# Optimization experiments

Measured on AMD Instinct MI355X. Metric: run time of the kernel, lower is better.

The kernel has to match this reference:

```python
import jax, jax.numpy as jnp
import numpy as np

DIM = 64
NUM_GRAPHS = 256
SLOPE = 11.0 / 48.0  # RReLU eval slope = ((1/8)+(1/3))/2
EPS = 1e-5


def _bn(x, g, b):
    m = x.mean(0)
    v = x.var(0)  # biased, matches torch BN normalization
    return (x - m) * jax.lax.rsqrt(v + EPS) * g + b


def _rrelu(x):
    return jnp.where(x >= 0, x, SLOPE * x)


def _gru(x, h, Wih, Whh, bih, bhh):
    gi = x @ Wih.T + bih
    gh = h @ Whh.T + bhh
    ir, iz, inn = jnp.split(gi, 3, -1)
    hr, hz, hn = jnp.split(gh, 3, -1)
    r = jax.nn.sigmoid(ir + hr)
    z = jax.nn.sigmoid(iz + hz)
    n = jnp.tanh(inn + r * hn)
    return (1.0 - z) * n + z * h


def _nnconv(x, ei, We, bias, n_nodes):
    # edge-conditioned conv: gather src, per-edge matmul, scatter-mean to dst
    src, dst = ei[0], ei[1]
    msg = jnp.einsum('ei,eio->eo', x[src], We)
    s = jax.ops.segment_sum(msg, dst, num_segments=n_nodes)
    cnt = jax.ops.segment_sum(jnp.ones((ei.shape[1],), x.dtype), dst, num_segments=n_nodes)
    return s / jnp.maximum(cnt, 1.0)[:, None] + bias


def _seg_softmax(e, seg, nseg):
    m = jax.ops.segment_max(e, seg, num_segments=nseg)
    ex = jnp.exp(e - m[seg])
    den = jax.ops.segment_sum(ex, seg, num_segments=nseg)
    return ex / den[seg]


def _set2set(x, seg, nseg, Wih, Whh, bih, bhh, steps=3):
    H = x.shape[-1]
    q_star = jnp.zeros((nseg, 2 * H), x.dtype)
    h = jnp.zeros((nseg, H), x.dtype)
    c = jnp.zeros((nseg, H), x.dtype)
    for _ in range(steps):
        gates = q_star @ Wih.T + bih + h @ Whh.T + bhh
        i, f, g, o = jnp.split(gates, 4, -1)
        c = jax.nn.sigmoid(f) * c + jax.nn.sigmoid(i) * jnp.tanh(g)
        h = jax.nn.sigmoid(o) * jnp.tanh(c)
        e = jnp.sum(x * h[seg], -1)
        a = _seg_softmax(e, seg, nseg)
        r = jax.ops.segment_sum(a[:, None] * x, seg, num_segments=nseg)
        q_star = jnp.concatenate([h, r], -1)
    return q_star


def reference(x, edge_index, edge_attr, edge_index3, edge_attr3, batch,
              bnx_g, bnx_b, Wn, bnode, We, be, Wnn1, bias1,
              Wih1, Whh1, bih1, bhh1, bnc_g, bnc_b, Wc1, bc1, Wc2, bc2,
              Wnn2, bias2, Wih2, Whh2, bih2, bhh2,
              Ws_ih, Ws_hh, bs_ih, bs_hh, bno_g, bno_b, Ww, Wb):
    N = x.shape[0]
    out = _rrelu(_bn(x, bnx_g, bnx_b) @ Wn + bnode)          # [N, 64]
    ea = _rrelu(edge_attr @ We + be)                          # [E, 12]
    W1 = (ea @ Wnn1).reshape(-1, DIM, DIM)                    # [E, 64, 64]
    h = out
    for _ in range(2):
        m = _rrelu(_nnconv(out, edge_index, W1, bias1, N))
        h = _gru(m, h, Wih1, Whh1, bih1, bhh1)
        out = h
    out = _bn(out, bnc_g, bnc_b)
    out = _rrelu(out @ Wc1 + bc1)
    out = _rrelu(out @ Wc2 + bc2)                             # [N, 128] (dropout=identity in eval)
    ei3s = jnp.concatenate([edge_index3, edge_index3[::-1]], axis=1)
    ea3s = jnp.concatenate([edge_attr3, edge_attr3], axis=0)
    W2 = (ea3s @ Wnn2).reshape(-1, 2 * DIM, 2 * DIM)          # [2*E3, 128, 128]
    h = out
    for _ in range(2):
        m = _rrelu(_nnconv(out, ei3s, W2, bias2, N))
        h = _gru(m, h, Wih2, Whh2, bih2, bhh2)
        out = h
    cbi = batch[edge_index3[0]]
    pool = _set2set(out, batch, NUM_GRAPHS, Ws_ih, Ws_hh, bs_ih, bs_hh)[cbi]
    t0 = out[edge_index3[0]]
    t1 = out[edge_index3[1]]
    yhat = jnp.concatenate([(t0 + t1) * 0.5, t0 * t1, (t0 - t1) ** 2, pool], axis=1)  # [E3, 640]
    yhat = _bn(yhat, bno_g, bno_b)
    w = edge_attr3 @ Ww
    b = edge_attr3 @ Wb
    return jnp.sum(yhat * w, axis=1) + b[:, 0]


def setup_inputs() -> dict:
    key = jax.random.key(0)
    ks = iter(jax.random.split(key, 64))
    def nrm(shape, scale=1.0):
        return jax.random.normal(next(ks), shape, jnp.float32) * scale
    def lin(i, o):
        return nrm((i, o), 1.0 / np.sqrt(i))
    N, E, E3 = 8192, 16384, 1024
    inp = {}
    inp['x'] = nrm((N, 8))
    inp['edge_index'] = jax.random.randint(next(ks), (2, E), 0, N)
    inp['edge_attr'] = nrm((E, 19))
    inp['edge_index3'] = jax.random.randint(next(ks), (2, E3), 0, N)
    inp['edge_attr3'] = nrm((E3, 8))
    inp['batch'] = jnp.repeat(jnp.arange(NUM_GRAPHS), N // NUM_GRAPHS)
    inp['bnx_g'] = jnp.ones(8); inp['bnx_b'] = jnp.zeros(8)
    inp['Wn'] = lin(8, 64); inp['bnode'] = jnp.zeros(64)
    inp['We'] = lin(19, 12); inp['be'] = jnp.zeros(12)
    inp['Wnn1'] = lin(12, DIM * DIM) * 0.5; inp['bias1'] = jnp.zeros(64)
    inp['Wih1'] = nrm((192, 64), 1.0 / np.sqrt(64)); inp['Whh1'] = nrm((192, 64), 1.0 / np.sqrt(64))
    inp['bih1'] = jnp.zeros(192); inp['bhh1'] = jnp.zeros(192)
    inp['bnc_g'] = jnp.ones(64); inp['bnc_b'] = jnp.zeros(64)
    inp['Wc1'] = lin(64, 128); inp['bc1'] = jnp.zeros(128)
    inp['Wc2'] = lin(128, 128); inp['bc2'] = jnp.zeros(128)
    inp['Wnn2'] = lin(8, 4 * DIM * DIM) * 0.5; inp['bias2'] = jnp.zeros(128)
    inp['Wih2'] = nrm((384, 128), 1.0 / np.sqrt(128)); inp['Whh2'] = nrm((384, 128), 1.0 / np.sqrt(128))
    inp['bih2'] = jnp.zeros(384); inp['bhh2'] = jnp.zeros(384)
    inp['Ws_ih'] = nrm((512, 256), 1.0 / np.sqrt(256)); inp['Ws_hh'] = nrm((512, 128), 1.0 / np.sqrt(128))
    inp['bs_ih'] = jnp.zeros(512); inp['bs_hh'] = jnp.zeros(512)
    inp['bno_g'] = jnp.ones(640); inp['bno_b'] = jnp.zeros(640)
    inp['Ww'] = lin(8, 640); inp['Wb'] = lin(8, 1)
    return inp
```

## Files before the change

kernel.cpp:

```cpp
#include <hip/hip_runtime.h>
#include <hip/hip_bf16.h>
#include <math.h>

#define N_NODES 8192
#define N_EDGES 16384
#define N_E3    1024
#define NGRAPH  256
#define NPG     32
#define SLOPE   (11.0f/48.0f)
#define BN_EPS  1e-5f

__device__ __forceinline__ float rrelu(float v){ return v >= 0.f ? v : SLOPE*v; }
__device__ __forceinline__ float sigm(float v){ return 1.f/(1.f+__expf(-v)); }

typedef _Float16 f16;
typedef __attribute__((ext_vector_type(8))) _Float16 half8v;
typedef __attribute__((ext_vector_type(4))) float f32x4;

__device__ __forceinline__ void zero_tail(int zb, float* zptr, int zcount) {
  float4 z4 = make_float4(0.f,0.f,0.f,0.f);
  int bd = blockDim.x;
  for (int i = zb*bd + (int)threadIdx.x; i*4 < zcount; i += 16*bd)
    ((float4*)zptr)[i] = z4;
}

__global__ __launch_bounds__(256) void conv1f_k(const float* __restrict__ nodeA,
    const int* __restrict__ ei, const float* __restrict__ ea,
    const f16* __restrict__ Wz1h, float* __restrict__ sbuf) {
  int t = threadIdx.x, lane = t & 63, wv = t >> 6;
  int e0 = blockIdx.x*64 + wv*16;
  int eA = e0 + (lane & 15);
  int src = ei[eA];
  int kb0 = (lane >> 4) * 8;
  const float* ap = nodeA + (size_t)src*64 + kb0;
  float4 v0 = *(const float4*)ap,      v1 = *(const float4*)(ap+4);
  float4 v2 = *(const float4*)(ap+32), v3 = *(const float4*)(ap+36);
  half8v a0, a1;
  a0[0]=(f16)v0.x; a0[1]=(f16)v0.y; a0[2]=(f16)v0.z; a0[3]=(f16)v0.w;
  a0[4]=(f16)v1.x; a0[5]=(f16)v1.y; a0[6]=(f16)v1.z; a0[7]=(f16)v1.w;
  a1[0]=(f16)v2.x; a1[1]=(f16)v2.y; a1[2]=(f16)v2.z; a1[3]=(f16)v2.w;
  a1[4]=(f16)v3.x; a1[5]=(f16)v3.y; a1[6]=(f16)v3.z; a1[7]=(f16)v3.w;
  float eav[12];
  #pragma unroll
  for (int kg = 0; kg < 12; kg++) eav[kg] = ea[eA*12 + kg];

  f32x4 acc[4] = {{0,0,0,0},{0,0,0,0},{0,0,0,0},{0,0,0,0}};
  #pragma unroll
  for (int kg = 0; kg < 12; kg++) {
    f16 s = (f16)eav[kg];
    half8v s0, s1;
    #pragma unroll
    for (int u = 0; u < 8; u++) { s0[u] = a0[u]*s; s1[u] = a1[u]*s; }
    #pragma unroll
    for (int jf = 0; jf < 4; jf++) {
      const f16* wp = Wz1h + (size_t)(kg*64 + jf*16 + (lane & 15))*64 + kb0;
      acc[jf] = __builtin_amdgcn_mfma_f32_16x16x32_f16(s0, *(const half8v*)wp, acc[jf], 0, 0, 0);
      acc[jf] = __builtin_amdgcn_mfma_f32_16x16x32_f16(s1, *(const half8v*)(wp+32), acc[jf], 0, 0, 0);
    }
  }
  int dstv[4];
  #pragma unroll
  for (int r = 0; r < 4; r++) dstv[r] = ei[N_EDGES + e0 + ((lane>>4)<<2) + r];
  #pragma unroll
  for (int jf = 0; jf < 4; jf++) {
    int col = jf*16 + (lane & 15);
    #pragma unroll
    for (int r = 0; r < 4; r++)
      atomicAdd(&sbuf[dstv[r]*64 + col], acc[jf][r]);
  }
}

__global__ __launch_bounds__(512) void conv2f_k(const float* __restrict__ nodeB,
    const int* __restrict__ ei3, const float* __restrict__ ea3,
    const f16* __restrict__ W2fh, float* __restrict__ sbuf) {
  int t = threadIdx.x, lane = t & 63, wv = t >> 6;
  int eg = blockIdx.x >> 1, qh = blockIdx.x & 1;
  int kgh = wv >> 2, jp = wv & 3;
  int e0 = eg * 16;
  int eA = e0 + (lane & 15);
  int src = ei3[eA];
  int kb0 = qh*64 + (lane >> 4) * 8;
  const float* ap = nodeB + (size_t)src*128 + kb0;
  half8v a0, a1;
  {
    float4 w0 = *(const float4*)ap,        w1 = *(const float4*)(ap+4);
    float4 w2 = *(const float4*)(ap + 32), w3 = *(const float4*)(ap+36);
    a0[0]=(f16)w0.x; a0[1]=(f16)w0.y; a0[2]=(f16)w0.z; a0[3]=(f16)w0.w;
    a0[4]=(f16)w1.x; a0[5]=(f16)w1.y; a0[6]=(f16)w1.z; a0[7]=(f16)w1.w;
    a1[0]=(f16)w2.x; a1[1]=(f16)w2.y; a1[2]=(f16)w2.z; a1[3]=(f16)w2.w;
    a1[4]=(f16)w3.x; a1[5]=(f16)w3.y; a1[6]=(f16)w3.z; a1[7]=(f16)w3.w;
  }
  int eb = eA & (N_E3 - 1);
  float eav[4];
  #pragma unroll
  for (int kk = 0; kk < 4; kk++) eav[kk] = ea3[eb*8 + kgh*4 + kk];

  f32x4 acc[2] = {{0,0,0,0},{0,0,0,0}};
  #pragma unroll
  for (int kk = 0; kk < 4; kk++) {
    f16 s = (f16)eav[kk];
    half8v s0, s1;
    #pragma unroll
    for (int u = 0; u < 8; u++) { s0[u] = a0[u]*s; s1[u] = a1[u]*s; }
    int kg = kgh*4 + kk;
    #pragma unroll
    for (int jj = 0; jj < 2; jj++) {
      int jf = jp*2 + jj;
      const f16* wp = W2fh + (size_t)(kg*128 + jf*16 + (lane & 15))*128 + kb0;
      acc[jj] = __builtin_amdgcn_mfma_f32_16x16x32_f16(s0, *(const half8v*)wp, acc[jj], 0, 0, 0);
      acc[jj] = __builtin_amdgcn_mfma_f32_16x16x32_f16(s1, *(const half8v*)(wp+32), acc[jj], 0, 0, 0);
    }
  }
  int dstv[4];
  #pragma unroll
  for (int r = 0; r < 4; r++) dstv[r] = ei3[(e0 + ((lane>>4)<<2) + r + N_E3) & (2*N_E3 - 1)];
  #pragma unroll
  for (int jj = 0; jj < 2; jj++) {
    int col = (jp*2+jj)*16 + (lane & 15);
    #pragma unroll
    for (int r = 0; r < 4; r++)
      atomicAdd(&sbuf[dstv[r]*128 + col], acc[jj][r]);
  }
}

template<int LOGH, int STATS>
__global__ void gruf_k(const float* __restrict__ sbuf, const float* __restrict__ cnt,
                       const float* __restrict__ mbias,
                       const f16* __restrict__ Wih, const f16* __restrict__ Whh,
                       const float* __restrict__ bih, const float* __restrict__ bhh,
                       const float* __restrict__ hold, float* __restrict__ hnew,
                       float* __restrict__ bns1, float* __restrict__ bns2,
                       int nblk, float* __restrict__ zptr, int zcount) {
  if ((int)blockIdx.x >= nblk) { zero_tail(blockIdx.x - nblk, zptr, zcount); return; }
  const int H = 1 << LOGH;
  const int K = H;
  const int jt = H >> 6;
  int t = threadIdx.x;
  int lane = t & 63, wv = t >> 6;
  int wpb = blockDim.x >> 6;
  int bm = blockIdx.x / jt, bj = blockIdx.x % jt;
  int n0 = bm * (wpb << 4) + (wv << 4);
  int j0 = bj << 6;
  int row = n0 + (lane & 15);
  int kb0 = (lane >> 4) * 8;

  f32x4 aR[4]  = {{0,0,0,0},{0,0,0,0},{0,0,0,0},{0,0,0,0}};
  f32x4 aZ[4]  = {{0,0,0,0},{0,0,0,0},{0,0,0,0},{0,0,0,0}};
  f32x4 aIN[4] = {{0,0,0,0},{0,0,0,0},{0,0,0,0},{0,0,0,0}};
  f32x4 aHN[4] = {{0,0,0,0},{0,0,0,0},{0,0,0,0},{0,0,0,0}};

  float dn = 1.f / fmaxf(cnt[row], 1.0f);
  for (int k0 = 0; k0 < K; k0 += 32) {
    int kb = k0 + kb0;
    const float* ap = sbuf + (size_t)row * K + kb;
    float4 v0 = *(const float4*)ap, v1 = *(const float4*)(ap + 4);
    float4 b0 = *(const float4*)(mbias + kb), b1 = *(const float4*)(mbias + kb + 4);
    half8v af;
    af[0]=(f16)rrelu(v0.x*dn+b0.x); af[1]=(f16)rrelu(v0.y*dn+b0.y);
    af[2]=(f16)rrelu(v0.z*dn+b0.z); af[3]=(f16)rrelu(v0.w*dn+b0.w);
    af[4]=(f16)rrelu(v1.x*dn+b1.x); af[5]=(f16)rrelu(v1.y*dn+b1.y);
    af[6]=(f16)rrelu(v1.z*dn+b1.z); af[7]=(f16)rrelu(v1.w*dn+b1.w);
    #pragma unroll
    for (int jf = 0; jf < 4; jf++) {
      int wr = j0 + jf*16 + (lane & 15);
      half8v wR = *(const half8v*)(Wih + (size_t)wr*K + kb);
      half8v wZ = *(const half8v*)(Wih + (size_t)(H + wr)*K + kb);
      half8v wN = *(const half8v*)(Wih + (size_t)(2*H + wr)*K + kb);
      aR[jf]  = __builtin_amdgcn_mfma_f32_16x16x32_f16(af, wR, aR[jf], 0, 0, 0);
      aZ[jf]  = __builtin_amdgcn_mfma_f32_16x16x32_f16(af, wZ, aZ[jf], 0, 0, 0);
      aIN[jf] = __builtin_amdgcn_mfma_f32_16x16x32_f16(af, wN, aIN[jf], 0, 0, 0);
    }
  }
  for (int k0 = 0; k0 < K; k0 += 32) {
    int kb = k0 + kb0;
    const float* ap = hold + (size_t)row * K + kb;
    float4 v0 = *(const float4*)ap, v1 = *(const float4*)(ap + 4);
    half8v af;
    af[0]=(f16)v0.x; af[1]=(f16)v0.y; af[2]=(f16)v0.z; af[3]=(f16)v0.w;
    af[4]=(f16)v1.x; af[5]=(f16)v1.y; af[6]=(f16)v1.z; af[7]=(f16)v1.w;
    #pragma unroll
    for (int jf = 0; jf < 4; jf++) {
      int wr = j0 + jf*16 + (lane & 15);
      half8v wR = *(const half8v*)(Whh + (size_t)wr*K + kb);
      half8v wZ = *(const half8v*)(Whh + (size_t)(H + wr)*K + kb);
      half8v wN = *(const half8v*)(Whh + (size_t)(2*H + wr)*K + kb);
      aR[jf]  = __builtin_amdgcn_mfma_f32_16x16x32_f16(af, wR, aR[jf], 0, 0, 0);
      aZ[jf]  = __builtin_amdgcn_mfma_f32_16x16x32_f16(af, wZ, aZ[jf], 0, 0, 0);
      aHN[jf] = __builtin_amdgcn_mfma_f32_16x16x32_f16(af, wN, aHN[jf], 0, 0, 0);
    }
  }
  int r0 = n0 + ((lane >> 4) << 2);
  #pragma unroll
  for (int jf = 0; jf < 4; jf++) {
    int col = j0 + jf*16 + (lane & 15);
    float bR = bih[col] + bhh[col];
    float bZ = bih[H + col] + bhh[H + col];
    float bI = bih[2*H + col], bH = bhh[2*H + col];
    float ssum = 0.f, sq = 0.f;
    #pragma unroll
    for (int r = 0; r < 4; r++) {
      float rr = sigm(aR[jf][r] + bR);
      float zz = sigm(aZ[jf][r] + bZ);
      float nn = tanhf(aIN[jf][r] + bI + rr*(aHN[jf][r] + bH));
      float ho = hold[(size_t)(r0 + r)*H + col];
      float hv = (1.f - zz)*nn + zz*ho;
      hnew[(size_t)(r0 + r)*H + col] = hv;
      if (STATS) { ssum += hv; sq += hv*hv; }
    }
    if (STATS) {
      ssum += __shfl_xor(ssum, 16); ssum += __shfl_xor(ssum, 32);
      sq   += __shfl_xor(sq, 16);   sq   += __shfl_xor(sq, 32);
      if (lane < 16) { atomicAdd(&bns1[col], ssum); atomicAdd(&bns2[col], sq); }
    }
  }
}

__global__ __launch_bounds__(256) void fcf_k(const float* __restrict__ A,
    const f16* __restrict__ W1, const float* __restrict__ b1v,
    const f16* __restrict__ W2, const float* __restrict__ b2v,
    const float* __restrict__ bns1, const float* __restrict__ bns2,
    const float* __restrict__ g, const float* __restrict__ b,
    float* __restrict__ outB,
    int nblk, float* __restrict__ zptr, int zcount) {
  if ((int)blockIdx.x >= nblk) { zero_tail(blockIdx.x - nblk, zptr, zcount); return; }
  __shared__ f16 y1s[4][16][128];
  int t = threadIdx.x, lane = t & 63, wv = t >> 6;
  int n0 = blockIdx.x*64 + wv*16;
  int row = n0 + (lane & 15);
  int kb0 = (lane >> 4) * 8;
  const float invN = 1.f / (float)N_NODES;

  const float* ap = A + (size_t)row*64 + kb0;
  half8v af0, af1;
  #pragma unroll
  for (int u = 0; u < 8; u++) {
    int k0i = kb0 + u, k1i = 32 + kb0 + u;
    float m0 = bns1[k0i]*invN, m1 = bns1[k1i]*invN;
    float va0 = bns2[k0i]*invN - m0*m0, va1 = bns2[k1i]*invN - m1*m1;
    af0[u] = (f16)((ap[u]    - m0)*rsqrtf(va0+BN_EPS)*g[k0i] + b[k0i]);
    af1[u] = (f16)((ap[32+u] - m1)*rsqrtf(va1+BN_EPS)*g[k1i] + b[k1i]);
  }
  f32x4 acc1[8] = {{0,0,0,0},{0,0,0,0},{0,0,0,0},{0,0,0,0},
                   {0,0,0,0},{0,0,0,0},{0,0,0,0},{0,0,0,0}};
  #pragma unroll
  for (int jf = 0; jf < 8; jf++) {
    const f16* wp = W1 + (size_t)(jf*16 + (lane & 15))*64 + kb0;
    acc1[jf] = __builtin_amdgcn_mfma_f32_16x16x32_f16(af0, *(const half8v*)wp, acc1[jf], 0, 0, 0);
    acc1[jf] = __builtin_amdgcn_mfma_f32_16x16x32_f16(af1, *(const half8v*)(wp+32), acc1[jf], 0, 0, 0);
  }
  #pragma unroll
  for (int jf = 0; jf < 8; jf++) {
    int col = jf*16 + (lane & 15);
    float bv = b1v[col];
    #pragma unroll
    for (int r = 0; r < 4; r++) {
      int rl = ((lane >> 4) << 2) + r;
      y1s[wv][rl][col] = (f16)rrelu(acc1[jf][r] + bv);
    }
  }
  __syncthreads();
  half8v bf[4];
  #pragma unroll
  for (int q = 0; q < 4; q++)
    bf[q] = *(const half8v*)&y1s[wv][lane & 15][q*32 + kb0];
  f32x4 acc2[8] = {{0,0,0,0},{0,0,0,0},{0,0,0,0},{0,0,0,0},
                   {0,0,0,0},{0,0,0,0},{0,0,0,0},{0,0,0,0}};
  #pragma unroll
  for (int jf = 0; jf < 8; jf++) {
    const f16* wp = W2 + (size_t)(jf*16 + (lane & 15))*128 + kb0;
    #pragma unroll
    for (int q = 0; q < 4; q++)
      acc2[jf] = __builtin_amdgcn_mfma_f32_16x16x32_f16(bf[q], *(const half8v*)(wp + q*32), acc2[jf], 0, 0, 0);
  }
  int r0 = n0 + ((lane >> 4) << 2);
  #pragma unroll
  for (int jf = 0; jf < 8; jf++) {
    int col = jf*16 + (lane & 15);
    float bv = b2v[col];
    #pragma unroll
    for (int r = 0; r < 4; r++)
      outB[(size_t)(r0 + r)*128 + col] = rrelu(acc2[jf][r] + bv);
  }
}

__global__ void bn_stats_k(const float* __restrict__ X, int nrow, int F,
                           float* __restrict__ mean, float* __restrict__ var) {
  int f = blockIdx.x, t = threadIdx.x;
  __shared__ float s1[256], s2[256];
  float a = 0.f, b = 0.f;
  for (int n = t; n < nrow; n += 256) {
    float v = X[(size_t)n * F + f];
    a += v; b += v * v;
  }
  s1[t] = a; s2[t] = b; __syncthreads();
  for (int w = 128; w > 0; w >>= 1) {
    if (t < w) { s1[t] += s1[t+w]; s2[t] += s2[t+w]; }
    __syncthreads();
  }
  if (t == 0) {
    float m = s1[0] / (float)nrow;
    mean[f] = m;
    var[f]  = s2[0] / (float)nrow - m * m;
  }
}

__global__ void embed_k(const float* __restrict__ x,
                        const float* __restrict__ mean, const float* __restrict__ var,
                        const float* __restrict__ g, const float* __restrict__ b,
                        const float* __restrict__ Wn, const float* __restrict__ bnode,
                        float* __restrict__ nodeA,
                        const float* __restrict__ eattr,
                        const float* __restrict__ We, const float* __restrict__ be,
                        float* __restrict__ ea12,
                        const int* __restrict__ ei, const int* __restrict__ ei3,
                        float* __restrict__ cnt1, float* __restrict__ cnt2,
                        float* __restrict__ zptr) {
  int bid = blockIdx.x, t = threadIdx.x;
  if (bid < 2048) {
    int idx = bid * 256 + t;
    int n = idx >> 6, o = idx & 63;
    float acc = bnode[o];
    #pragma unroll
    for (int i = 0; i < 8; i++) {
      float xn = (x[n*8+i] - mean[i]) * rsqrtf(var[i] + BN_EPS) * g[i] + b[i];
      acc += xn * Wn[i*64 + o];
    }
    nodeA[idx] = rrelu(acc);
  } else if (bid < 2816) {
    int idx = (bid - 2048) * 256 + t;
    if (idx >= N_EDGES * 12) return;
    int e = idx / 12, j = idx - e * 12;
    float acc = be[j];
    #pragma unroll
    for (int k = 0; k < 19; k++) acc += eattr[e*19+k] * We[k*12 + j];
    ea12[idx] = rrelu(acc);
  } else if (bid < 2880) {
    int idx = (bid - 2816) * 256 + t;
    if (idx < N_EDGES) atomicAdd(&cnt1[ei[N_EDGES + idx]], 1.0f);
    if (idx < N_E3) {
      atomicAdd(&cnt2[ei3[N_E3 + idx]], 1.0f);
      atomicAdd(&cnt2[ei3[idx]], 1.0f);
    }
  } else {
    zero_tail(bid - 2880, zptr, N_NODES*64);
  }
}

__global__ void pack_k(const float* __restrict__ Wnn1,
                       const float* __restrict__ Wih1, const float* __restrict__ Whh1,
                       const float* __restrict__ Wc1,  const float* __restrict__ Wc2,
                       const float* __restrict__ Wnn2,
                       const float* __restrict__ Wih2, const float* __restrict__ Whh2,
                       const float* __restrict__ Ws_ih, const float* __restrict__ Ws_hh,
                       f16* __restrict__ Wz1h,
                       f16* __restrict__ Wih1h, f16* __restrict__ Whh1h,
                       f16* __restrict__ Wc1Th, f16* __restrict__ Wc2Th,
                       f16* __restrict__ W2fh,
                       f16* __restrict__ Wih2h, f16* __restrict__ Whh2h,
                       float* __restrict__ Wfold,
                       float* __restrict__ cnt1, float* __restrict__ cnt2,
                       float* __restrict__ bns1, float* __restrict__ bns2) {
  int idx = blockIdx.x * 256 + threadIdx.x;
  if (idx < 49152) {
    int jj = idx >> 6, i = idx & 63;
    int k = jj >> 6, o = jj & 63;
    Wz1h[idx] = (f16)Wnn1[k*4096 + i*64 + o];
  }
  if (idx < 12288) { Wih1h[idx] = (f16)Wih1[idx]; Whh1h[idx] = (f16)Whh1[idx]; }
  if (idx < 8192) {
    int o = idx >> 6, i = idx & 63;
    Wc1Th[idx] = (f16)Wc1[i*128 + o];
  }
  if (idx < 16384) {
    int o = idx >> 7, i = idx & 127;
    Wc2Th[idx] = (f16)Wc2[i*128 + o];
  }
  if (idx < 131072) {
    int r = idx >> 7, i = idx & 127;
    int k = r >> 7, o = r & 127;
    W2fh[idx] = (f16)Wnn2[k*16384 + i*128 + o];
  }
  if (idx < 49152) { Wih2h[idx] = (f16)Wih2[idx]; Whh2h[idx] = (f16)Whh2[idx]; }
  if (idx < 131072) {
    int i = idx >> 9, j = idx & 511;
    float v = Ws_ih[(size_t)j*256 + i];
    if (i < 128) v += Ws_hh[(size_t)j*128 + i];
    Wfold[idx] = v;
  }
  if (idx < N_NODES) { cnt1[idx] = 0.f; cnt2[idx] = 0.f; }
  if (idx < 128) { bns1[idx] = 0.f; bns2[idx] = 0.f; }
}

__global__ __launch_bounds__(1024) void set2set_k(const float* __restrict__ x,
    const float* __restrict__ Wfold,
    const float* __restrict__ bs_ih, const float* __restrict__ bs_hh,
    float* __restrict__ qpool) {
  int g = blockIdx.x, t = threadIdx.x;
  __shared__ float xs[NPG*128];
  __shared__ float hr[256];
  __shared__ float cbuf[128];
  __shared__ float pbuf[1024];
  __shared__ float abuf[NPG];
  *(float4*)&xs[t*4] = *(const float4*)(x + (size_t)g*NPG*128 + t*4);
  if (t < 128) {
    float gi = bs_ih[t]     + bs_hh[t];
    float gg = bs_ih[256+t] + bs_hh[256+t];
    float go = bs_ih[384+t] + bs_hh[384+t];
    float c0 = sigm(gi) * tanhf(gg);
    cbuf[t] = c0;
    hr[t] = sigm(go) * tanhf(c0);
  }
  __syncthreads();
  #pragma unroll 1
  for (int step = 0; step < 3; step++) {
    {
      int node = t >> 5, s = t & 31;
      const float* xr = xs + node*128 + s*4;
      float p = xr[0]*hr[s*4] + xr[1]*hr[s*4+1] + xr[2]*hr[s*4+2] + xr[3]*hr[s*4+3];
      p += __shfl_down(p, 16, 32); p += __shfl_down(p, 8, 32);
      p += __shfl_down(p, 4, 32);  p += __shfl_down(p, 2, 32);
      p += __shfl_down(p, 1, 32);
      if (s == 0) pbuf[node] = p;
    }
    __syncthreads();
    if (t < NPG) {
      float e = pbuf[t];
      float mx = e;
      for (int o = 16; o > 0; o >>= 1) mx = fmaxf(mx, __shfl_xor(mx, o, 32));
      float ex = __expf(e - mx);
      float den = ex;
      for (int o = 16; o > 0; o >>= 1) den += __shfl_xor(den, o, 32);
      abuf[t] = ex / den;
    }
    __syncthreads();
    if (t < 128) {
      float r = 0.f;
      #pragma unroll 8
      for (int nn = 0; nn < NPG; nn++) r += abuf[nn] * xs[nn*128 + t];
      hr[128 + t] = r;
    }
    __syncthreads();
    if (step == 2) break;
    {
      int j = t & 511, half = t >> 9;
      const float* wp = Wfold + (size_t)(half*128)*512 + j;
      const float* iv = hr + half*128;
      float a0=0.f, a1=0.f, a2=0.f, a3=0.f;
      #pragma unroll 4
      for (int i = 0; i < 128; i += 4) {
        a0 += iv[i]   * wp[(i)  *512];
        a1 += iv[i+1] * wp[(i+1)*512];
        a2 += iv[i+2] * wp[(i+2)*512];
        a3 += iv[i+3] * wp[(i+3)*512];
      }
      pbuf[t] = a0 + a1 + a2 + a3;
    }
    __syncthreads();
    if (t < 128) {
      float gi = pbuf[t]     + pbuf[512+t] + bs_ih[t]     + bs_hh[t];
      float gf = pbuf[128+t] + pbuf[640+t] + bs_ih[128+t] + bs_hh[128+t];
      float gg = pbuf[256+t] + pbuf[768+t] + bs_ih[256+t] + bs_hh[256+t];
      float go = pbuf[384+t] + pbuf[896+t] + bs_ih[384+t] + bs_hh[384+t];
      float ci = sigm(gf) * cbuf[t] + sigm(gi) * tanhf(gg);
      cbuf[t] = ci;
      hr[t] = sigm(go) * tanhf(ci);
    }
    __syncthreads();
  }
  if (t < 256) qpool[g*256 + t] = hr[t];
}

__global__ void yhat_k(const float* __restrict__ feat, const int* __restrict__ ei3,
                       const int* __restrict__ batch, const float* __restrict__ qpool,
                       float* __restrict__ yhat) {
  int idx = blockIdx.x * blockDim.x + threadIdx.x;
  if (idx >= N_E3 * 640) return;
  int e = idx / 640, j = idx - e * 640;
  int s0 = ei3[e], s1 = ei3[N_E3 + e];
  float v;
  if (j < 128)      { v = 0.5f * (feat[s0*128+j] + feat[s1*128+j]); }
  else if (j < 256) { int jj = j-128; v = feat[s0*128+jj] * feat[s1*128+jj]; }
  else if (j < 384) { int jj = j-256; float d = feat[s0*128+jj] - feat[s1*128+jj]; v = d*d; }
  else              { int cbi = batch[s0]; v = qpool[cbi*256 + (j-384)]; }
  yhat[idx] = v;
}

__global__ void final_k(const float* __restrict__ yhat,
                        const float* __restrict__ mean, const float* __restrict__ var,
                        const float* __restrict__ g, const float* __restrict__ b,
                        const float* __restrict__ ea3,
                        const float* __restrict__ Ww, const float* __restrict__ Wb,
                        float* __restrict__ out) {
  int e = blockIdx.x, t = threadIdx.x;
  __shared__ float red[128];
  float av[8];
  #pragma unroll
  for (int k = 0; k < 8; k++) av[k] = ea3[e*8 + k];
  float acc = 0.f;
  for (int j = t; j < 640; j += 128) {
    float yn = (yhat[(size_t)e*640 + j] - mean[j]) * rsqrtf(var[j] + BN_EPS) * g[j] + b[j];
    float wj = 0.f;
    #pragma unroll
    for (int k = 0; k < 8; k++) wj += av[k] * Ww[k*640 + j];
    acc += yn * wj;
  }
  red[t] = acc; __syncthreads();
  for (int w = 64; w > 0; w >>= 1) {
    if (t < w) red[t] += red[t+w];
    __syncthreads();
  }
  if (t == 0) {
    float bb = 0.f;
    #pragma unroll
    for (int k = 0; k < 8; k++) bb += av[k] * Wb[k];
    out[e] = red[0] + bb;
  }
}

extern "C" void kernel_launch(void* const* d_in, const int* in_sizes, int n_in,
                              void* d_out, int out_size, void* d_ws, size_t ws_size,
                              hipStream_t stream) {
  const float* x      = (const float*)d_in[0];
  const int*   ei     = (const int*)  d_in[1];
  const float* eattr  = (const float*)d_in[2];
  const int*   ei3    = (const int*)  d_in[3];
  const float* ea3    = (const float*)d_in[4];
  const int*   batch  = (const int*)  d_in[5];
  const float* bnx_g  = (const float*)d_in[6];
  const float* bnx_b  = (const float*)d_in[7];
  const float* Wn     = (const float*)d_in[8];
  const float* bnode  = (const float*)d_in[9];
  const float* We     = (const float*)d_in[10];
  const float* be     = (const float*)d_in[11];
  const float* Wnn1   = (const float*)d_in[12];
  const float* bias1  = (const float*)d_in[13];
  const float* Wih1   = (const float*)d_in[14];
  const float* Whh1   = (const float*)d_in[15];
  const float* bih1   = (const float*)d_in[16];
  const float* bhh1   = (const float*)d_in[17];
  const float* bnc_g  = (const float*)d_in[18];
  const float* bnc_b  = (const float*)d_in[19];
  const float* Wc1    = (const float*)d_in[20];
  const float* bc1    = (const float*)d_in[21];
  const float* Wc2    = (const float*)d_in[22];
  const float* bc2    = (const float*)d_in[23];
  const float* Wnn2   = (const float*)d_in[24];
  const float* bias2  = (const float*)d_in[25];
  const float* Wih2   = (const float*)d_in[26];
  const float* Whh2   = (const float*)d_in[27];
  const float* bih2   = (const float*)d_in[28];
  const float* bhh2   = (const float*)d_in[29];
  const float* Ws_ih  = (const float*)d_in[30];
  const float* Ws_hh  = (const float*)d_in[31];
  const float* bs_ih  = (const float*)d_in[32];
  const float* bs_hh  = (const float*)d_in[33];
  const float* bno_g  = (const float*)d_in[34];
  const float* bno_b  = (const float*)d_in[35];
  const float* Ww     = (const float*)d_in[36];
  const float* Wb     = (const float*)d_in[37];
  float* out = (float*)d_out;

  float* W = (float*)d_ws;
  size_t off = 0;
  float* Wfold  = W + off; off += 131072;
  float* ea12   = W + off; off += (size_t)N_EDGES * 12;
  float* nodeA  = W + off; off += (size_t)N_NODES * 64;
  float* nodeA2 = W + off; off += (size_t)N_NODES * 64;
  float* sA1    = W + off; off += (size_t)N_NODES * 64;
  float* sA2    = W + off; off += (size_t)N_NODES * 64;
  float* sB1    = W + off; off += (size_t)N_NODES * 128;
  float* sB2    = W + off; off += (size_t)N_NODES * 128;
  float* cnt1   = W + off; off += (size_t)N_NODES;
  float* cnt2   = W + off; off += (size_t)N_NODES;
  float* nodeB  = W + off; off += (size_t)N_NODES * 128;
  float* nodeB2 = W + off; off += (size_t)N_NODES * 128;
  float* qpool  = W + off; off += (size_t)NGRAPH * 256;
  float* yhat   = W + off; off += (size_t)N_E3 * 640;
  float* mean   = W + off; off += 640;
  float* var    = W + off; off += 640;
  float* bns1   = W + off; off += 128;
  float* bns2   = W + off; off += 128;
  f16* F = (f16*)(W + off);
  size_t foff = 0;
  f16* Wz1h  = F + foff; foff += 49152;
  f16* Wih1h = F + foff; foff += 12288;
  f16* Whh1h = F + foff; foff += 12288;
  f16* Wc1Th = F + foff; foff += 8192;
  f16* Wc2Th = F + foff; foff += 16384;
  f16* W2fh  = F + foff; foff += 131072;
  f16* Wih2h = F + foff; foff += 49152;
  f16* Whh2h = F + foff; foff += 49152;
  (void)foff; (void)ws_size; (void)in_sizes; (void)n_in; (void)out_size;

  pack_k<<<512, 256, 0, stream>>>(Wnn1, Wih1, Whh1, Wc1, Wc2, Wnn2, Wih2, Whh2, Ws_ih, Ws_hh,
                                  Wz1h, Wih1h, Whh1h, Wc1Th, Wc2Th, W2fh, Wih2h, Whh2h,
                                  Wfold, cnt1, cnt2, bns1, bns2);
  bn_stats_k<<<8, 256, 0, stream>>>(x, N_NODES, 8, mean, var);
  embed_k<<<2896, 256, 0, stream>>>(x, mean, var, bnx_g, bnx_b, Wn, bnode, nodeA,
                                    eattr, We, be, ea12, ei, ei3, cnt1, cnt2, sA1);

  conv1f_k<<<256, 256, 0, stream>>>(nodeA, ei, ea12, Wz1h, sA1);
  gruf_k<6,0><<<272, 128, 0, stream>>>(sA1, cnt1, bias1, Wih1h, Whh1h, bih1, bhh1,
                                       nodeA, nodeA2, nullptr, nullptr,
                                       256, sA2, N_NODES*64);
  conv1f_k<<<256, 256, 0, stream>>>(nodeA2, ei, ea12, Wz1h, sA2);
  gruf_k<6,1><<<272, 128, 0, stream>>>(sA2, cnt1, bias1, Wih1h, Whh1h, bih1, bhh1,
                                       nodeA2, nodeA, bns1, bns2,
                                       256, sB1, N_NODES*128);

  fcf_k<<<144, 256, 0, stream>>>(nodeA, Wc1Th, bc1, Wc2Th, bc2,
                                 bns1, bns2, bnc_g, bnc_b, nodeB,
                                 128, sB2, N_NODES*128);

  conv2f_k<<<256, 512, 0, stream>>>(nodeB, ei3, ea3, W2fh, sB1);
  gruf_k<7,0><<<256, 256, 0, stream>>>(sB1, cnt2, bias2, Wih2h, Whh2h, bih2, bhh2,
                                       nodeB, nodeB2, nullptr, nullptr,
                                       256, nullptr, 0);
  conv2f_k<<<256, 512, 0, stream>>>(nodeB2, ei3, ea3, W2fh, sB2);
  gruf_k<7,0><<<256, 256, 0, stream>>>(sB2, cnt2, bias2, Wih2h, Whh2h, bih2, bhh2,
                                       nodeB2, nodeB, nullptr, nullptr,
                                       256, nullptr, 0);

  set2set_k<<<NGRAPH, 1024, 0, stream>>>(nodeB, Wfold, bs_ih, bs_hh, qpool);

  yhat_k<<<(N_E3*640 + 255)/256, 256, 0, stream>>>(nodeB, ei3, batch, qpool, yhat);
  bn_stats_k<<<640, 256, 0, stream>>>(yhat, N_E3, 640, mean, var);
  final_k<<<N_E3, 128, 0, stream>>>(yhat, mean, var, bno_g, bno_b, ea3, Ww, Wb, out);
}
```

Baseline: 198.7 us.

## Fuse pack, embed, conv and GRU stages into one cooperative persistent kernel

Replaces the chain of about eleven small launches (weight packing, BN stats, embedding, two conv1/GRU rounds, FC, two conv2/GRU rounds) with one cooperative kernel of 256 blocks of 512 threads that separates the stages with grid.sync. The goal is to remove kernel launch gaps and tail effects between many short stages. Work is remapped to fewer, larger blocks with 8 waves each, so some stages now run on only part of the grid. Grid-wide barriers carry their own cost, and the 512-thread blocks with launch_bounds(512,2) may limit register use for the MFMA bodies.

```diff
diff --git a/kernel.cpp b/kernel.cpp
--- a/kernel.cpp
+++ b/kernel.cpp
@@ -1,6 +1,9 @@
 #include <hip/hip_runtime.h>
+#include <hip/hip_cooperative_groups.h>
 #include <hip/hip_bf16.h>
 #include <math.h>
+
+namespace cg = cooperative_groups;
 
 #define N_NODES 8192
 #define N_EDGES 16384
@@ -17,18 +20,29 @@
 typedef __attribute__((ext_vector_type(8))) _Float16 half8v;
 typedef __attribute__((ext_vector_type(4))) float f32x4;
 
-__device__ __forceinline__ void zero_tail(int zb, float* zptr, int zcount) {
+struct P {
+  const float *x, *eattr, *ea3;
+  const int *ei, *ei3;
+  const float *bnx_g, *bnx_b, *Wn, *bnode, *We, *be;
+  const float *Wnn1, *bias1, *Wih1, *Whh1, *bih1, *bhh1;
+  const float *bnc_g, *bnc_b, *Wc1, *bc1, *Wc2, *bc2;
+  const float *Wnn2, *bias2, *Wih2, *Whh2, *bih2, *bhh2;
+  const float *Ws_ih, *Ws_hh;
+  float *mean, *var, *ea12, *nodeA, *nodeA2, *sA1, *sA2, *sB1, *sB2;
+  float *cnt1, *cnt2, *nodeB, *nodeB2, *bns1, *bns2, *Wfold;
+  f16 *Wz1h, *Wih1h, *Whh1h, *Wc1Th, *Wc2Th, *W2fh, *Wih2h, *Whh2h;
+};
+
+__device__ __forceinline__ void zero_block(int zb, float* zptr, int zcount) {
   float4 z4 = make_float4(0.f,0.f,0.f,0.f);
-  int bd = blockDim.x;
-  for (int i = zb*bd + (int)threadIdx.x; i*4 < zcount; i += 16*bd)
+  for (int i = zb*512 + (int)threadIdx.x; i*4 < zcount; i += 16*512)
     ((float4*)zptr)[i] = z4;
 }
 
-__global__ __launch_bounds__(256) void conv1f_k(const float* __restrict__ nodeA,
-    const int* __restrict__ ei, const float* __restrict__ ea,
-    const f16* __restrict__ Wz1h, float* __restrict__ sbuf) {
-  int t = threadIdx.x, lane = t & 63, wv = t >> 6;
-  int e0 = blockIdx.x*64 + wv*16;
+__device__ void conv1f_body(const float* __restrict__ nodeA, const int* __restrict__ ei,
+    const float* __restrict__ ea, const f16* __restrict__ Wz1h, float* __restrict__ sbuf,
+    int blk, int lane, int wv) {
+  int e0 = blk*128 + wv*16;
   int eA = e0 + (lane & 15);
   int src = ei[eA];
   int kb0 = (lane >> 4) * 8;
@@ -43,7 +57,6 @@
   float eav[12];
   #pragma unroll
   for (int kg = 0; kg < 12; kg++) eav[kg] = ea[eA*12 + kg];
-
   f32x4 acc[4] = {{0,0,0,0},{0,0,0,0},{0,0,0,0},{0,0,0,0}};
   #pragma unroll
   for (int kg = 0; kg < 12; kg++) {
@@ -70,11 +83,10 @@
   }
 }
 
-__global__ __launch_bounds__(512) void conv2f_k(const float* __restrict__ nodeB,
-    const int* __restrict__ ei3, const float* __restrict__ ea3,
-    const f16* __restrict__ W2fh, float* __restrict__ sbuf) {
-  int t = threadIdx.x, lane = t & 63, wv = t >> 6;
-  int eg = blockIdx.x >> 1, qh = blockIdx.x & 1;
+__device__ void conv2f_body(const float* __restrict__ nodeB, const int* __restrict__ ei3,
+    const float* __restrict__ ea3, const f16* __restrict__ W2fh, float* __restrict__ sbuf,
+    int blk, int lane, int wv) {
+  int eg = blk >> 1, qh = blk & 1;
   int kgh = wv >> 2, jp = wv & 3;
   int e0 = eg * 16;
   int eA = e0 + (lane & 15);
@@ -94,7 +106,6 @@
   float eav[4];
   #pragma unroll
   for (int kk = 0; kk < 4; kk++) eav[kk] = ea3[eb*8 + kgh*4 + kk];
-
   f32x4 acc[2] = {{0,0,0,0},{0,0,0,0}};
   #pragma unroll
   for (int kk = 0; kk < 4; kk++) {
@@ -124,22 +135,18 @@
 }
 
 template<int LOGH, int STATS>
-__global__ void gruf_k(const float* __restrict__ sbuf, const float* __restrict__ cnt,
-                       const float* __restrict__ mbias,
-                       const f16* __restrict__ Wih, const f16* __restrict__ Whh,
-                       const float* __restrict__ bih, const float* __restrict__ bhh,
-                       const float* __restrict__ hold, float* __restrict__ hnew,
-                       float* __restrict__ bns1, float* __restrict__ bns2,
-                       int nblk, float* __restrict__ zptr, int zcount) {
-  if ((int)blockIdx.x >= nblk) { zero_tail(blockIdx.x - nblk, zptr, zcount); return; }
+__device__ void gruf_body(const float* __restrict__ sbuf, const float* __restrict__ cnt,
+    const float* __restrict__ mbias,
+    const f16* __restrict__ Wih, const f16* __restrict__ Whh,
+    const float* __restrict__ bih, const float* __restrict__ bhh,
+    const float* __restrict__ hold, float* __restrict__ hnew,
+    float* __restrict__ bns1, float* __restrict__ bns2,
+    int blk, int lane, int wv) {
   const int H = 1 << LOGH;
   const int K = H;
   const int jt = H >> 6;
-  int t = threadIdx.x;
-  int lane = t & 63, wv = t >> 6;
-  int wpb = blockDim.x >> 6;
-  int bm = blockIdx.x / jt, bj = blockIdx.x % jt;
-  int n0 = bm * (wpb << 4) + (wv << 4);
+  int bm = blk / jt, bj = blk % jt;
+  int n0 = bm * 128 + wv * 16;
   int j0 = bj << 6;
   int row = n0 + (lane & 15);
   int kb0 = (lane >> 4) * 8;
@@ -215,17 +222,14 @@
   }
 }
 
-__global__ __launch_bounds__(256) void fcf_k(const float* __restrict__ A,
+__device__ void fcf_body(const float* __restrict__ A,
     const f16* __restrict__ W1, const float* __restrict__ b1v,
     const f16* __restrict__ W2, const float* __restrict__ b2v,
     const float* __restrict__ bns1, const float* __restrict__ bns2,
     const float* __restrict__ g, const float* __restrict__ b,
-    float* __restrict__ outB,
-    int nblk, float* __restrict__ zptr, int zcount) {
-  if ((int)blockIdx.x >= nblk) { zero_tail(blockIdx.x - nblk, zptr, zcount); return; }
-  __shared__ f16 y1s[4][16][128];
-  int t = threadIdx.x, lane = t & 63, wv = t >> 6;
-  int n0 = blockIdx.x*64 + wv*16;
+    float* __restrict__ outB, int blk, int lane, int wv) {
+  __shared__ f16 y1s[8][16][128];
+  int n0 = blk*128 + wv*16;
   int row = n0 + (lane & 15);
   int kb0 = (lane >> 4) * 8;
   const float invN = 1.f / (float)N_NODES;
@@ -281,6 +285,124 @@
     for (int r = 0; r < 4; r++)
       outB[(size_t)(r0 + r)*128 + col] = rrelu(acc2[jf][r] + bv);
   }
+}
+
+__global__ __launch_bounds__(512, 2) void coop_k(P p) {
+  cg::grid_group grid = cg::this_grid();
+  int blk = blockIdx.x, t = threadIdx.x;
+  int lane = t & 63, wv = t >> 6;
+
+  if (blk == 0) {
+    if (wv < 8) {
+      float s = 0.f, q = 0.f;
+      for (int n = lane; n < N_NODES; n += 64) {
+        float v = p.x[n*8 + wv];
+        s += v; q += v*v;
+      }
+      #pragma unroll
+      for (int o = 32; o > 0; o >>= 1) { s += __shfl_xor(s, o); q += __shfl_xor(q, o); }
+      if (lane == 0) {
+        float m = s / (float)N_NODES;
+        p.mean[wv] = m;
+        p.var[wv]  = q / (float)N_NODES - m*m;
+      }
+    }
+  } else {
+    for (int idx = (blk-1)*512 + t; idx < 131072; idx += 255*512) {
+      if (idx < 49152) {
+        int jj = idx >> 6, i = idx & 63;
+        int k = jj >> 6, o = jj & 63;
+        p.Wz1h[idx] = (f16)p.Wnn1[k*4096 + i*64 + o];
+        p.Wih1h[idx < 12288 ? idx : 0] = (f16)p.Wih1[idx < 12288 ? idx : 0];
+      }
+      if (idx < 12288) p.Whh1h[idx] = (f16)p.Whh1[idx];
+      if (idx < 8192) {
+        int o = idx >> 6, i = idx & 63;
+        p.Wc1Th[idx] = (f16)p.Wc1[i*128 + o];
+      }
+      if (idx < 16384) {
+        int o = idx >> 7, i = idx & 127;
+        p.Wc2Th[idx] = (f16)p.Wc2[i*128 + o];
+      }
+      if (idx < 131072) {
+        int r = idx >> 7, i = idx & 127;
+        int k = r >> 7, o = r & 127;
+        p.W2fh[idx] = (f16)p.Wnn2[k*16384 + i*128 + o];
+      }
+      if (idx < 49152) { p.Wih2h[idx] = (f16)p.Wih2[idx]; p.Whh2h[idx] = (f16)p.Whh2[idx]; }
+      if (idx < 131072) {
+        int i = idx >> 9, j = idx & 511;
+        float v = p.Ws_ih[(size_t)j*256 + i];
+        if (i < 128) v += p.Ws_hh[(size_t)j*128 + i];
+        p.Wfold[idx] = v;
+      }
+      if (idx < N_NODES) { p.cnt1[idx] = 0.f; p.cnt2[idx] = 0.f; }
+      if (idx < 128) { p.bns1[idx] = 0.f; p.bns2[idx] = 0.f; }
+      if (idx < 131072) ((float4*)p.sA1)[idx] = make_float4(0.f,0.f,0.f,0.f);
+    }
+  }
+  grid.sync();
+
+  {
+    int gtid = blk*512 + t;
+    for (int idx = gtid; idx < N_NODES*64; idx += 131072) {
+      int n = idx >> 6, o = idx & 63;
+      float acc = p.bnode[o];
+      #pragma unroll
+      for (int i = 0; i < 8; i++) {
+        float xn = (p.x[n*8+i] - p.mean[i]) * rsqrtf(p.var[i] + BN_EPS) * p.bnx_g[i] + p.bnx_b[i];
+        acc += xn * p.Wn[i*64 + o];
+      }
+      p.nodeA[idx] = rrelu(acc);
+    }
+    for (int idx = gtid; idx < N_EDGES*12; idx += 131072) {
+      int e = idx / 12, j = idx - e * 12;
+      float acc = p.be[j];
+      #pragma unroll
+      for (int k = 0; k < 19; k++) acc += p.eattr[e*19+k] * p.We[k*12 + j];
+      p.ea12[idx] = rrelu(acc);
+    }
+    if (gtid < N_EDGES) atomicAdd(&p.cnt1[p.ei[N_EDGES + gtid]], 1.0f);
+    if (gtid < N_E3) {
+      atomicAdd(&p.cnt2[p.ei3[N_E3 + gtid]], 1.0f);
+      atomicAdd(&p.cnt2[p.ei3[gtid]], 1.0f);
+    }
+  }
+  grid.sync();
+
+  if (blk < 128) conv1f_body(p.nodeA, p.ei, p.ea12, p.Wz1h, p.sA1, blk, lane, wv);
+  else if (blk < 144) zero_block(blk - 128, p.sA2, N_NODES*64);
+  grid.sync();
+
+  if (blk < 64) gruf_body<6,0>(p.sA1, p.cnt1, p.bias1, p.Wih1h, p.Whh1h, p.bih1, p.bhh1,
+                               p.nodeA, p.nodeA2, nullptr, nullptr, blk, lane, wv);
+  else if (blk < 80) zero_block(blk - 64, p.sB1, N_NODES*128);
+  grid.sync();
+
+  if (blk < 128) conv1f_body(p.nodeA2, p.ei, p.ea12, p.Wz1h, p.sA2, blk, lane, wv);
+  else if (blk < 144) zero_block(blk - 128, p.sB2, N_NODES*128);
+  grid.sync();
+
+  if (blk < 64) gruf_body<6,1>(p.sA2, p.cnt1, p.bias1, p.Wih1h, p.Whh1h, p.bih1, p.bhh1,
+                               p.nodeA2, p.nodeA, p.bns1, p.bns2, blk, lane, wv);
+  grid.sync();
+
+  if (blk < 64) fcf_body(p.nodeA, p.Wc1Th, p.bc1, p.Wc2Th, p.bc2,
+                         p.bns1, p.bns2, p.bnc_g, p.bnc_b, p.nodeB, blk, lane, wv);
+  grid.sync();
+
+  conv2f_body(p.nodeB, p.ei3, p.ea3, p.W2fh, p.sB1, blk, lane, wv);
+  grid.sync();
+
+  if (blk < 128) gruf_body<7,0>(p.sB1, p.cnt2, p.bias2, p.Wih2h, p.Whh2h, p.bih2, p.bhh2,
+                                p.nodeB, p.nodeB2, nullptr, nullptr, blk, lane, wv);
+  grid.sync();
+
+  conv2f_body(p.nodeB2, p.ei3, p.ea3, p.W2fh, p.sB2, blk, lane, wv);
+  grid.sync();
+
+  if (blk < 128) gruf_body<7,0>(p.sB2, p.cnt2, p.bias2, p.Wih2h, p.Whh2h, p.bih2, p.bhh2,
+                                p.nodeB2, p.nodeB, nullptr, nullptr, blk, lane, wv);
 }
 
 __global__ void bn_stats_k(const float* __restrict__ X, int nrow, int F,
@@ -302,93 +424,6 @@
     mean[f] = m;
     var[f]  = s2[0] / (float)nrow - m * m;
   }
-}
-
-__global__ void embed_k(const float* __restrict__ x,
-                        const float* __restrict__ mean, const float* __restrict__ var,
-                        const float* __restrict__ g, const float* __restrict__ b,
-                        const float* __restrict__ Wn, const float* __restrict__ bnode,
-                        float* __restrict__ nodeA,
-                        const float* __restrict__ eattr,
-                        const float* __restrict__ We, const float* __restrict__ be,
-                        float* __restrict__ ea12,
-                        const int* __restrict__ ei, const int* __restrict__ ei3,
-                        float* __restrict__ cnt1, float* __restrict__ cnt2,
-                        float* __restrict__ zptr) {
-  int bid = blockIdx.x, t = threadIdx.x;
-  if (bid < 2048) {
-    int idx = bid * 256 + t;
-    int n = idx >> 6, o = idx & 63;
-    float acc = bnode[o];
-    #pragma unroll
-    for (int i = 0; i < 8; i++) {
-      float xn = (x[n*8+i] - mean[i]) * rsqrtf(var[i] + BN_EPS) * g[i] + b[i];
-      acc += xn * Wn[i*64 + o];
-    }
-    nodeA[idx] = rrelu(acc);
-  } else if (bid < 2816) {
-    int idx = (bid - 2048) * 256 + t;
-    if (idx >= N_EDGES * 12) return;
-    int e = idx / 12, j = idx - e * 12;
-    float acc = be[j];
-    #pragma unroll
-    for (int k = 0; k < 19; k++) acc += eattr[e*19+k] * We[k*12 + j];
-    ea12[idx] = rrelu(acc);
-  } else if (bid < 2880) {
-    int idx = (bid - 2816) * 256 + t;
-    if (idx < N_EDGES) atomicAdd(&cnt1[ei[N_EDGES + idx]], 1.0f);
-    if (idx < N_E3) {
-      atomicAdd(&cnt2[ei3[N_E3 + idx]], 1.0f);
-      atomicAdd(&cnt2[ei3[idx]], 1.0f);
-    }
-  } else {
-    zero_tail(bid - 2880, zptr, N_NODES*64);
-  }
-}
-
-__global__ void pack_k(const float* __restrict__ Wnn1,
-                       const float* __restrict__ Wih1, const float* __restrict__ Whh1,
-                       const float* __restrict__ Wc1,  const float* __restrict__ Wc2,
-                       const float* __restrict__ Wnn2,
-                       const float* __restrict__ Wih2, const float* __restrict__ Whh2,
-                       const float* __restrict__ Ws_ih, const float* __restrict__ Ws_hh,
-                       f16* __restrict__ Wz1h,
-                       f16* __restrict__ Wih1h, f16* __restrict__ Whh1h,
-                       f16* __restrict__ Wc1Th, f16* __restrict__ Wc2Th,
-                       f16* __restrict__ W2fh,
-                       f16* __restrict__ Wih2h, f16* __restrict__ Whh2h,
-                       float* __restrict__ Wfold,
-                       float* __restrict__ cnt1, float* __restrict__ cnt2,
-                       float* __restrict__ bns1, float* __restrict__ bns2) {
-  int idx = blockIdx.x * 256 + threadIdx.x;
-  if (idx < 49152) {
-    int jj = idx >> 6, i = idx & 63;
-    int k = jj >> 6, o = jj & 63;
-    Wz1h[idx] = (f16)Wnn1[k*4096 + i*64 + o];
-  }
-  if (idx < 12288) { Wih1h[idx] = (f16)Wih1[idx]; Whh1h[idx] = (f16)Whh1[idx]; }
-  if (idx < 8192) {
-    int o = idx >> 6, i = idx & 63;
-    Wc1Th[idx] = (f16)Wc1[i*128 + o];
-  }
-  if (idx < 16384) {
-    int o = idx >> 7, i = idx & 127;
-    Wc2Th[idx] = (f16)Wc2[i*128 + o];
-  }
-  if (idx < 131072) {
-    int r = idx >> 7, i = idx & 127;
-    int k = r >> 7, o = r & 127;
-    W2fh[idx] = (f16)Wnn2[k*16384 + i*128 + o];
-  }
-  if (idx < 49152) { Wih2h[idx] = (f16)Wih2[idx]; Whh2h[idx] = (f16)Whh2[idx]; }
-  if (idx < 131072) {
-    int i = idx >> 9, j = idx & 511;
-    float v = Ws_ih[(size_t)j*256 + i];
-    if (i < 128) v += Ws_hh[(size_t)j*128 + i];
-    Wfold[idx] = v;
-  }
-  if (idx < N_NODES) { cnt1[idx] = 0.f; cnt2[idx] = 0.f; }
-  if (idx < 128) { bns1[idx] = 0.f; bns2[idx] = 0.f; }
 }
 
 __global__ __launch_bounds__(1024) void set2set_k(const float* __restrict__ x,
@@ -416,11 +451,11 @@
     {
       int node = t >> 5, s = t & 31;
       const float* xr = xs + node*128 + s*4;
-      float p = xr[0]*hr[s*4] + xr[1]*hr[s*4+1] + xr[2]*hr[s*4+2] + xr[3]*hr[s*4+3];
-      p += __shfl_down(p, 16, 32); p += __shfl_down(p, 8, 32);
-      p += __shfl_down(p, 4, 32);  p += __shfl_down(p, 2, 32);
-      p += __shfl_down(p, 1, 32);
-      if (s == 0) pbuf[node] = p;
+      float pv = xr[0]*hr[s*4] + xr[1]*hr[s*4+1] + xr[2]*hr[s*4+2] + xr[3]*hr[s*4+3];
+      pv += __shfl_down(pv, 16, 32); pv += __shfl_down(pv, 8, 32);
+      pv += __shfl_down(pv, 4, 32);  pv += __shfl_down(pv, 2, 32);
+      pv += __shfl_down(pv, 1, 32);
+      if (s == 0) pbuf[node] = pv;
     }
     __syncthreads();
     if (t < NPG) {
@@ -592,37 +627,31 @@
   f16* Whh2h = F + foff; foff += 49152;
   (void)foff; (void)ws_size; (void)in_sizes; (void)n_in; (void)out_size;
 
-  pack_k<<<512, 256, 0, stream>>>(Wnn1, Wih1, Whh1, Wc1, Wc2, Wnn2, Wih2, Whh2, Ws_ih, Ws_hh,
-                                  Wz1h, Wih1h, Whh1h, Wc1Th, Wc2Th, W2fh, Wih2h, Whh2h,
-                                  Wfold, cnt1, cnt2, bns1, bns2);
-  bn_stats_k<<<8, 256, 0, stream>>>(x, N_NODES, 8, mean, var);
-  embed_k<<<2896, 256, 0, stream>>>(x, mean, var, bnx_g, bnx_b, Wn, bnode, nodeA,
-                                    eattr, We, be, ea12, ei, ei3, cnt1, cnt2, sA1);
-
-  conv1f_k<<<256, 256, 0, stream>>>(nodeA, ei, ea12, Wz1h, sA1);
-  gruf_k<6,0><<<272, 128, 0, stream>>>(sA1, cnt1, bias1, Wih1h, Whh1h, bih1, bhh1,
-                                       nodeA, nodeA2, nullptr, nullptr,
-                                       256, sA2, N_NODES*64);
-  conv1f_k<<<256, 256, 0, stream>>>(nodeA2, ei, ea12, Wz1h, sA2);
-  gruf_k<6,1><<<272, 128, 0, stream>>>(sA2, cnt1, bias1, Wih1h, Whh1h, bih1, bhh1,
-                                       nodeA2, nodeA, bns1, bns2,
-                                       256, sB1, N_NODES*128);
-
-  fcf_k<<<144, 256, 0, stream>>>(nodeA, Wc1Th, bc1, Wc2Th, bc2,
-                                 bns1, bns2, bnc_g, bnc_b, nodeB,
-                                 128, sB2, N_NODES*128);
-
-  conv2f_k<<<256, 512, 0, stream>>>(nodeB, ei3, ea3, W2fh, sB1);
-  gruf_k<7,0><<<256, 256, 0, stream>>>(sB1, cnt2, bias2, Wih2h, Whh2h, bih2, bhh2,
-                                       nodeB, nodeB2, nullptr, nullptr,
-                                       256, nullptr, 0);
-  conv2f_k<<<256, 512, 0, stream>>>(nodeB2, ei3, ea3, W2fh, sB2);
-  gruf_k<7,0><<<256, 256, 0, stream>>>(sB2, cnt2, bias2, Wih2h, Whh2h, bih2, bhh2,
-                                       nodeB2, nodeB, nullptr, nullptr,
-                                       256, nullptr, 0);
+  P prm;
+  prm.x = x; prm.eattr = eattr; prm.ea3 = ea3; prm.ei = ei; prm.ei3 = ei3;
+  prm.bnx_g = bnx_g; prm.bnx_b = bnx_b; prm.Wn = Wn; prm.bnode = bnode;
+  prm.We = We; prm.be = be;
+  prm.Wnn1 = Wnn1; prm.bias1 = bias1; prm.Wih1 = Wih1; prm.Whh1 = Whh1;
+  prm.bih1 = bih1; prm.bhh1 = bhh1;
+  prm.bnc_g = bnc_g; prm.bnc_b = bnc_b; prm.Wc1 = Wc1; prm.bc1 = bc1;
+  prm.Wc2 = Wc2; prm.bc2 = bc2;
+  prm.Wnn2 = Wnn2; prm.bias2 = bias2; prm.Wih2 = Wih2; prm.Whh2 = Whh2;
+  prm.bih2 = bih2; prm.bhh2 = bhh2;
+  prm.Ws_ih = Ws_ih; prm.Ws_hh = Ws_hh;
+  prm.mean = mean; prm.var = var; prm.ea12 = ea12;
+  prm.nodeA = nodeA; prm.nodeA2 = nodeA2;
+  prm.sA1 = sA1; prm.sA2 = sA2; prm.sB1 = sB1; prm.sB2 = sB2;
+  prm.cnt1 = cnt1; prm.cnt2 = cnt2;
+  prm.nodeB = nodeB; prm.nodeB2 = nodeB2;
+  prm.bns1 = bns1; prm.bns2 = bns2; prm.Wfold = Wfold;
+  prm.Wz1h = Wz1h; prm.Wih1h = Wih1h; prm.Whh1h = Whh1h;
+  prm.Wc1Th = Wc1Th; prm.Wc2Th = Wc2Th; prm.W2fh = W2fh;
+  prm.Wih2h = Wih2h; prm.Whh2h = Whh2h;
+
+  void* kargs[] = { (void*)&prm };
+  hipLaunchCooperativeKernel((const void*)coop_k, dim3(256), dim3(512), kargs, 0, stream);
 
   set2set_k<<<NGRAPH, 1024, 0, stream>>>(nodeB, Wfold, bs_ih, bs_hh, qpool);
-
   yhat_k<<<(N_E3*640 + 255)/256, 256, 0, stream>>>(nodeB, ei3, batch, qpool, yhat);
   bn_stats_k<<<640, 256, 0, stream>>>(yhat, N_E3, 640, mean, var);
   final_k<<<N_E3, 128, 0, stream>>>(yhat, mean, var, bno_g, bno_b, ea3, Ww, Wb, out);
```

Measured after the change: 538.8 us. 2.71x slower.
